# Performance work log

Measured on AMD Instinct MI355X. Metric: run time of the kernel, lower is better.

Reference implementation:

```python
import jax, jax.numpy as jnp
import numpy as np

FONT_NUM = 190
HID = 256
HEADS = 2
EPS = 1e-5


def _bn(x, g, b, m, v):
    # eval-mode BatchNorm over the last (channel) axis
    return (x - m) * (g * jax.lax.rsqrt(v + EPS)) + b


def _gru(x, Wih, Whh, bih, bhh):
    # x: [B, S, D]; PyTorch gate order r, z, n. Returns all hidden states [B, S, H].
    B, S, _ = x.shape
    H = Whh.shape[1]
    xp = x @ Wih.T + bih  # [B, S, 3H] -- one big GEMM for all timesteps
    def step(h, xt):
        gh = h @ Whh.T + bhh
        xr, xz, xn = jnp.split(xt, 3, axis=-1)
        hr, hz, hn = jnp.split(gh, 3, axis=-1)
        r = jax.nn.sigmoid(xr + hr)
        z = jax.nn.sigmoid(xz + hz)
        n = jnp.tanh(xn + r * hn)
        h_new = (1.0 - z) * n + z * h
        return h_new, h_new
    h0 = jnp.zeros((B, H), x.dtype)
    _, hs = jax.lax.scan(step, h0, jnp.swapaxes(xp, 0, 1))
    return jnp.swapaxes(hs, 0, 1)


def _forward(img_emb, text_embs, len_mask, label_mask, labels,
             img_W, img_b, img_g, img_beta, img_m, img_v,
             g1_Wih, g1_Whh, g1_bih, g1_bhh, tl_W, tl_b,
             t_g, t_beta, t_m, t_v,
             g2_Wih, g2_Whh, g2_bih, g2_bhh, cl_W, cl_b,
             c_g, c_beta, c_m, c_v,
             attn_Win, attn_bin, attn_Wout, attn_bout, pred_W, pred_b):
    # img encoder: Linear -> BN -> (Dropout eval=id) -> ReLU
    img_fea = jax.nn.relu(_bn(img_emb @ img_W.T + img_b, img_g, img_beta, img_m, img_v))  # [B,H]
    # text encoder: GRU -> ReLU -> Linear, then BN+ReLU (torch does this in [B,C,S]; equivalent over channels)
    t = jax.nn.relu(_gru(text_embs, g1_Wih, g1_Whh, g1_bih, g1_bhh))
    t = t @ tl_W.T + tl_b
    text_fea = jax.nn.relu(_bn(t, t_g, t_beta, t_m, t_v))  # [B,S,H]
    len_info = len_mask.sum(axis=1)  # [B]
    # NOTE: sum over ALL timesteps divided by valid length (faithful to source)
    mean = text_fea.sum(axis=1) / len_info[:, None]  # [B,H]
    contrast = text_fea - mean[:, None, :]
    c = jax.nn.relu(_gru(contrast, g2_Wih, g2_Whh, g2_bih, g2_bhh))
    c = c @ cl_W.T + cl_b
    contrast_fea = jax.nn.relu(_bn(c, c_g, c_beta, c_m, c_v))  # [B,S,H]
    B, S, H = text_fea.shape
    hd = H // HEADS
    # batched 3-token self-attention: collapse the per-timestep python loop into one call
    tokens = jnp.stack([
        jnp.broadcast_to(img_fea[:, None, :], (B, S, H)), text_fea, contrast_fea
    ], axis=0).reshape(3, B * S, H)  # [3, N, H]
    Wq, Wk, Wv = jnp.split(attn_Win, 3, axis=0)
    bq, bk, bv = jnp.split(attn_bin, 3, axis=0)
    scale = 1.0 / jnp.sqrt(jnp.asarray(hd, tokens.dtype))
    q = (tokens @ Wq.T + bq).reshape(3, B * S, HEADS, hd) * scale
    k = (tokens @ Wk.T + bk).reshape(3, B * S, HEADS, hd)
    v = (tokens @ Wv.T + bv).reshape(3, B * S, HEADS, hd)
    scores = jnp.einsum('tnhd,snhd->nhts', q, k)  # [N, heads, 3, 3]
    attn = jax.nn.softmax(scores, axis=-1)
    o = jnp.einsum('nhts,snhd->tnhd', attn, v).reshape(3, B * S, H)
    o = o @ attn_Wout.T + attn_bout
    last = o.mean(axis=0).reshape(B, S, H)  # att_fea.mean(0) over the 3 tokens
    logits = last @ pred_W.T + pred_b  # [B,S,FONT_NUM]
    pred = jax.nn.softmax(logits, axis=-1)
    oh = jnp.maximum(label_mask, jax.nn.one_hot(labels, FONT_NUM, dtype=pred.dtype))
    loss = -(oh * jnp.log(pred)).sum(axis=-1)  # [B,S]
    loss = (loss * len_mask).sum(axis=1) / len_info
    return loss.mean()


def setup_inputs() -> dict:
    key = jax.random.key(0)
    ks = jax.random.split(key, 16)
    B, S, D, H = 128, 128, 2048, HID
    img_emb = jax.random.normal(ks[0], (B, D), jnp.float32)
    text_embs = jax.random.normal(ks[1], (B, S, D), jnp.float32)
    lengths = jax.random.randint(ks[2], (B,), S // 2, S + 1)
    len_mask = (jnp.arange(S)[None, :] < lengths[:, None]).astype(jnp.float32)
    labels = jax.random.randint(ks[3], (B, S), 0, FONT_NUM)
    label_mask = jnp.zeros((B, S, FONT_NUM), jnp.float32)
    w = lambda k, sh: jax.random.normal(k, sh, jnp.float32) * 0.02
    params = dict(
        img_W=w(ks[4], (H, D)), img_b=jnp.zeros((H,)),
        img_g=jnp.ones((H,)), img_beta=jnp.zeros((H,)), img_m=jnp.zeros((H,)), img_v=jnp.ones((H,)),
        g1_Wih=w(ks[5], (3 * (H // 2), D)), g1_Whh=w(ks[6], (3 * (H // 2), H // 2)),
        g1_bih=jnp.zeros((3 * (H // 2),)), g1_bhh=jnp.zeros((3 * (H // 2),)),
        tl_W=w(ks[7], (H, H // 2)), tl_b=jnp.zeros((H,)),
        t_g=jnp.ones((H,)), t_beta=jnp.zeros((H,)), t_m=jnp.zeros((H,)), t_v=jnp.ones((H,)),
        g2_Wih=w(ks[8], (3 * H, H)), g2_Whh=w(ks[9], (3 * H, H)),
        g2_bih=jnp.zeros((3 * H,)), g2_bhh=jnp.zeros((3 * H,)),
        cl_W=w(ks[10], (H, H)), cl_b=jnp.zeros((H,)),
        c_g=jnp.ones((H,)), c_beta=jnp.zeros((H,)), c_m=jnp.zeros((H,)), c_v=jnp.ones((H,)),
        attn_Win=w(ks[11], (3 * H, H)), attn_bin=jnp.zeros((3 * H,)),
        attn_Wout=w(ks[12], (H, H)), attn_bout=jnp.zeros((H,)),
        pred_W=w(ks[13], (FONT_NUM, H)), pred_b=jnp.zeros((FONT_NUM,)),
    )
    return dict(img_emb=img_emb, text_embs=text_embs, len_mask=len_mask,
                label_mask=label_mask, labels=labels, **params)


def reference(img_emb, text_embs, len_mask, label_mask, labels,
              img_W, img_b, img_g, img_beta, img_m, img_v,
              g1_Wih, g1_Whh, g1_bih, g1_bhh, tl_W, tl_b,
              t_g, t_beta, t_m, t_v,
              g2_Wih, g2_Whh, g2_bih, g2_bhh, cl_W, cl_b,
              c_g, c_beta, c_m, c_v,
              attn_Win, attn_bin, attn_Wout, attn_bout, pred_W, pred_b):
    return _forward(img_emb, text_embs, len_mask, label_mask, labels,
                    img_W, img_b, img_g, img_beta, img_m, img_v,
                    g1_Wih, g1_Whh, g1_bih, g1_bhh, tl_W, tl_b,
                    t_g, t_beta, t_m, t_v,
                    g2_Wih, g2_Whh, g2_bih, g2_bhh, cl_W, cl_b,
                    c_g, c_beta, c_m, c_v,
                    attn_Win, attn_bin, attn_Wout, attn_bout, pred_W, pred_b)
```

## Files before the change

kernel.cpp:

```cpp
#include <hip/hip_runtime.h>

typedef __attribute__((ext_vector_type(8))) short short8;
typedef __attribute__((ext_vector_type(4))) float f32x4;
typedef _Float16 f16;
typedef __attribute__((ext_vector_type(2))) _Float16 f16x2;
typedef __attribute__((ext_vector_type(8))) _Float16 f16x8;

__device__ inline float bf2f(unsigned short u){
  union{float f; unsigned u32;} x; x.u32 = ((unsigned)u) << 16; return x.f;
}
__device__ inline unsigned short f2bf(float f){
  union{float f; unsigned u;} x; x.f = f;
  unsigned r = (x.u + 0x7FFFu + ((x.u >> 16) & 1u)) >> 16;
  return (unsigned short)r;
}

#if defined(__has_builtin)
#  if __has_builtin(__builtin_amdgcn_fdot2)
#    define HAS_FDOT2 1
#  endif
#endif
__device__ inline float dot2f(f16x2 a, f16x2 b, float c){
#ifdef HAS_FDOT2
  return __builtin_amdgcn_fdot2(a, b, c, false);
#else
  return c + (float)a.x * (float)b.x + (float)a.y * (float)b.y;
#endif
}
__device__ inline f16x2 asf16x2(int v){ return __builtin_bit_cast(f16x2, v); }
__device__ inline int pack2(float lo, float hi){
  f16x2 p = f16x2{(f16)lo, (f16)hi};
  return __builtin_bit_cast(int, p);
}

__device__ inline float sigmoidf_(float x){ return 1.f / (1.f + __expf(-x)); }
__device__ inline float tanh_fast(float x){ float e = __expf(2.f * x); return 1.f - 2.f / (e + 1.f); }

__device__ inline float dpp_xor1(float x){
  return __int_as_float(__builtin_amdgcn_update_dpp(0, __float_as_int(x), 0xB1, 0xF, 0xF, true));
}
__device__ inline float dpp_xor2(float x){
  return __int_as_float(__builtin_amdgcn_update_dpp(0, __float_as_int(x), 0x4E, 0xF, 0xF, true));
}

__device__ inline void load8bf(const unsigned short* p, float* o){
  uint4 q = *(const uint4*)p;
  o[0]=bf2f((unsigned short)(q.x & 0xffffu)); o[1]=bf2f((unsigned short)(q.x >> 16));
  o[2]=bf2f((unsigned short)(q.y & 0xffffu)); o[3]=bf2f((unsigned short)(q.y >> 16));
  o[4]=bf2f((unsigned short)(q.z & 0xffffu)); o[5]=bf2f((unsigned short)(q.z >> 16));
  o[6]=bf2f((unsigned short)(q.w & 0xffffu)); o[7]=bf2f((unsigned short)(q.w >> 16));
}

#define GLL16(g, l) __builtin_amdgcn_global_load_lds(                      \
    (const __attribute__((address_space(1))) void*)(g),                    \
    (__attribute__((address_space(3))) void*)(l), 16, 0, 0)

__global__ __launch_bounds__(256) void conv_bf16_k(const float* __restrict__ src,
                                                   unsigned short* __restrict__ dst, int n4){
  int i = blockIdx.x * 256 + threadIdx.x;
  if (i >= n4) return;
  float4 v = ((const float4*)src)[i];
  union { unsigned short s[4]; uint2 q; } u;
  u.s[0]=f2bf(v.x); u.s[1]=f2bf(v.y); u.s[2]=f2bf(v.z); u.s[3]=f2bf(v.w);
  ((uint2*)dst)[i] = u.q;
}

__global__ __launch_bounds__(256) void conv_f16_k(const float* __restrict__ src,
                                                  f16* __restrict__ dst, int n4){
  int i = blockIdx.x * 256 + threadIdx.x;
  if (i >= n4) return;
  float4 v = ((const float4*)src)[i];
  union { f16 s[4]; uint2 q; } u;
  u.s[0]=(f16)v.x; u.s[1]=(f16)v.y; u.s[2]=(f16)v.z; u.s[3]=(f16)v.w;
  ((uint2*)dst)[i] = u.q;
}

__global__ __launch_bounds__(256) void pred_pad_k(const float* __restrict__ W,
                                                  const float* __restrict__ b,
                                                  unsigned short* __restrict__ Wd,
                                                  float* __restrict__ bd){
  int i = blockIdx.x * 256 + threadIdx.x;
  int j = i >> 8;
  Wd[i] = (j < 190) ? f2bf(W[i]) : (unsigned short)0;
  if (i < 192) bd[i] = (i < 190) ? b[i] : 0.f;
}

template<int OUT_T, bool BN, bool AF32>
__global__ __launch_bounds__(256) void gemm128_k(
    const void* __restrict__ Ap, const unsigned short* __restrict__ Bw,
    const float* __restrict__ bias,
    const float* __restrict__ gam, const float* __restrict__ bet,
    const float* __restrict__ mu,  const float* __restrict__ var,
    void* __restrict__ Cp, int M, int N, int K)
{
  __shared__ __align__(16) unsigned short As[4096];
  __shared__ __align__(16) unsigned short Bs[4096];
  const int tid  = threadIdx.x;
  const int lane = tid & 63, wid = tid >> 6;
  const int wm = wid & 1, wn = wid >> 1;
  const int bm = blockIdx.y << 7, bn = blockIdx.x << 7;
  const int rA = tid >> 2, seg = tid & 3;

  f32x4 acc[4][4];
  #pragma unroll
  for (int i = 0; i < 4; i++)
    #pragma unroll
    for (int j = 0; j < 4; j++)
      acc[i][j] = f32x4{0.f, 0.f, 0.f, 0.f};

  const unsigned short* Abf = (const unsigned short*)Ap;
  const float* Af = (const float*)Ap;
  char* asb = (char*)As;
  char* bsb = (char*)Bs;
  char* asw = asb + wid * 1024;
  char* bsw = bsb + wid * 1024;

  for (int k0 = 0; k0 < K; k0 += 32) {
    if (AF32) {
      #pragma unroll
      for (int beta = 0; beta < 2; beta++) {
        const float* src = Af + (size_t)(bm + rA + beta * 64) * K + k0 + seg * 8;
        float4 v0 = *(const float4*)src;
        float4 v1 = *(const float4*)(src + 4);
        union { unsigned short s[8]; uint4 q; } u;
        u.s[0]=f2bf(v0.x); u.s[1]=f2bf(v0.y); u.s[2]=f2bf(v0.z); u.s[3]=f2bf(v0.w);
        u.s[4]=f2bf(v1.x); u.s[5]=f2bf(v1.y); u.s[6]=f2bf(v1.z); u.s[7]=f2bf(v1.w);
        *(uint4*)(asb + beta * 4096 + tid * 16) = u.q;
      }
    } else {
      GLL16(Abf + (size_t)(bm + rA)      * K + k0 + seg * 8, asw);
      GLL16(Abf + (size_t)(bm + rA + 64) * K + k0 + seg * 8, asw + 4096);
    }
    GLL16(Bw + (size_t)(bn + rA)      * K + k0 + seg * 8, bsw);
    GLL16(Bw + (size_t)(bn + rA + 64) * K + k0 + seg * 8, bsw + 4096);
    __syncthreads();

    short8 a[4], b[4];
    #pragma unroll
    for (int f = 0; f < 4; f++) {
      int ra = wm * 64 + f * 16 + (lane & 15);
      a[f] = *(const short8*)(asb + ra * 64 + (lane >> 4) * 16);
      int rb = wn * 64 + f * 16 + (lane & 15);
      b[f] = *(const short8*)(bsb + rb * 64 + (lane >> 4) * 16);
    }
    #pragma unroll
    for (int fm = 0; fm < 4; fm++)
      #pragma unroll
      for (int fn = 0; fn < 4; fn++)
        acc[fm][fn] = __builtin_amdgcn_mfma_f32_16x16x32_bf16(a[fm], b[fn], acc[fm][fn], 0, 0, 0);
    __syncthreads();
  }

  #pragma unroll
  for (int fn = 0; fn < 4; fn++) {
    int col = bn + wn * 64 + fn * 16 + (lane & 15);
    float bs = bias[col];
    float sc = 1.f, sh = 0.f;
    if (BN) { float s = gam[col] * rsqrtf(var[col] + 1e-5f); sc = s; sh = bet[col] - mu[col] * s; }
    #pragma unroll
    for (int fm = 0; fm < 4; fm++) {
      int row = bm + wm * 64 + fm * 16 + ((lane >> 4) << 2);
      #pragma unroll
      for (int j = 0; j < 4; j++) {
        float v = acc[fm][fn][j] + bs;
        if (BN) { v = v * sc + sh; v = fmaxf(v, 0.f); }
        size_t idx = (size_t)(row + j) * N + col;
        if (OUT_T == 1) ((f16*)Cp)[idx] = (f16)v;
        else            ((unsigned short*)Cp)[idx] = f2bf(v);
      }
    }
  }
}

template<int OUT_T, bool BN, bool AF32>
__global__ __launch_bounds__(256) void gemm_k(
    const void* __restrict__ Ap, const unsigned short* __restrict__ Bw,
    const float* __restrict__ bias,
    const float* __restrict__ gam, const float* __restrict__ bet,
    const float* __restrict__ mu,  const float* __restrict__ var,
    void* __restrict__ Cp, int M, int N, int K)
{
  __shared__ unsigned short As[64][40];
  __shared__ unsigned short Bs[64][40];
  const int tid  = threadIdx.x;
  const int lane = tid & 63, wid = tid >> 6;
  const int wm = wid & 1, wn = wid >> 1;
  const int bm = blockIdx.y << 6, bn = blockIdx.x << 6;
  const int srow = tid >> 2, sseg = tid & 3;

  f32x4 acc[2][2];
  #pragma unroll
  for (int i = 0; i < 2; i++)
    #pragma unroll
    for (int j = 0; j < 2; j++)
      acc[i][j] = f32x4{0.f, 0.f, 0.f, 0.f};

  const unsigned short* Abf = (const unsigned short*)Ap;
  const float* Af = (const float*)Ap;

  for (int k0 = 0; k0 < K; k0 += 32) {
    if (AF32) {
      const float* src = Af + (size_t)(bm + srow) * K + k0 + sseg * 8;
      float4 v0 = *(const float4*)(src);
      float4 v1 = *(const float4*)(src + 4);
      union { unsigned short s[8]; uint4 q; } u;
      u.s[0]=f2bf(v0.x); u.s[1]=f2bf(v0.y); u.s[2]=f2bf(v0.z); u.s[3]=f2bf(v0.w);
      u.s[4]=f2bf(v1.x); u.s[5]=f2bf(v1.y); u.s[6]=f2bf(v1.z); u.s[7]=f2bf(v1.w);
      *(uint4*)&As[srow][sseg * 8] = u.q;
    } else {
      *(uint4*)&As[srow][sseg * 8] =
          *(const uint4*)(Abf + (size_t)(bm + srow) * K + k0 + sseg * 8);
    }
    *(uint4*)&Bs[srow][sseg * 8] =
        *(const uint4*)(Bw + (size_t)(bn + srow) * K + k0 + sseg * 8);
    __syncthreads();

    short8 a0 = *(const short8*)&As[wm * 32 +      (lane & 15)][(lane >> 4) * 8];
    short8 a1 = *(const short8*)&As[wm * 32 + 16 + (lane & 15)][(lane >> 4) * 8];
    short8 b0 = *(const short8*)&Bs[wn * 32 +      (lane & 15)][(lane >> 4) * 8];
    short8 b1 = *(const short8*)&Bs[wn * 32 + 16 + (lane & 15)][(lane >> 4) * 8];
    acc[0][0] = __builtin_amdgcn_mfma_f32_16x16x32_bf16(a0, b0, acc[0][0], 0, 0, 0);
    acc[0][1] = __builtin_amdgcn_mfma_f32_16x16x32_bf16(a0, b1, acc[0][1], 0, 0, 0);
    acc[1][0] = __builtin_amdgcn_mfma_f32_16x16x32_bf16(a1, b0, acc[1][0], 0, 0, 0);
    acc[1][1] = __builtin_amdgcn_mfma_f32_16x16x32_bf16(a1, b1, acc[1][1], 0, 0, 0);
    __syncthreads();
  }

  #pragma unroll
  for (int fn = 0; fn < 2; fn++) {
    int col = bn + wn * 32 + fn * 16 + (lane & 15);
    float bs = bias[col];
    float sc = 1.f, sh = 0.f;
    if (BN) { float s = gam[col] * rsqrtf(var[col] + 1e-5f); sc = s; sh = bet[col] - mu[col] * s; }
    #pragma unroll
    for (int fm = 0; fm < 2; fm++) {
      int row = bm + wm * 32 + fm * 16 + ((lane >> 4) << 2);
      #pragma unroll
      for (int j = 0; j < 4; j++) {
        float v = acc[fm][fn][j] + bs;
        if (BN) { v = v * sc + sh; v = fmaxf(v, 0.f); }
        size_t idx = (size_t)(row + j) * N + col;
        if (OUT_T == 0)      ((float*)Cp)[idx] = v;
        else if (OUT_T == 1) ((f16*)Cp)[idx]   = (f16)v;
        else                 ((unsigned short*)Cp)[idx] = f2bf(v);
      }
    }
  }
}

__global__ __launch_bounds__(512, 2) void gru2_scan_k(
    const f16* __restrict__ Wf,
    const float* __restrict__ bhh,
    const f16* __restrict__ xp, unsigned short* __restrict__ hs_relu)
{
  const int b = blockIdx.x;
  const int tid = threadIdx.x;
  const int jj = tid >> 1, kh = tid & 1;
  __shared__ __align__(16) f16 hbuf[2][256];
  __shared__ __align__(16) char wnl[16 * 512 * 16];

  {
    const f16* src = Wf + (size_t)(512 + jj) * 256 + kh * 128;
    #pragma unroll
    for (int c = 0; c < 16; c++)
      *(uint4*)(wnl + c * 8192 + tid * 16) = *(const uint4*)(src + c * 8);
  }

  int wri[64], wzi[64];
  #pragma unroll
  for (int i = 0; i < 16; i++) {
    const int kb = kh * 128 + i * 8;
    uint4 q;
    q = *(const uint4*)&Wf[(size_t)(jj      ) * 256 + kb];
    wri[4*i+0] = (int)q.x; wri[4*i+1] = (int)q.y; wri[4*i+2] = (int)q.z; wri[4*i+3] = (int)q.w;
    q = *(const uint4*)&Wf[(size_t)(jj + 256) * 256 + kb];
    wzi[4*i+0] = (int)q.x; wzi[4*i+1] = (int)q.y; wzi[4*i+2] = (int)q.z; wzi[4*i+3] = (int)q.w;
  }
  #pragma unroll
  for (int i = 0; i < 64; i++)
    asm volatile("" : "+v"(wri[i]), "+v"(wzi[i]));

  const float br = bhh[jj], bz = bhh[jj + 256], bn2 = bhh[jj + 512];
  if (tid < 256) hbuf[0][tid] = (f16)0.f;
  float hprev = 0.f;
  f16 pxr = (f16)0.f, pxz = (f16)0.f, pxn = (f16)0.f;
  if (kh == 0) {
    const f16* x0 = xp + (size_t)(b * 128) * 768;
    pxr = x0[jj]; pxz = x0[256 + jj]; pxn = x0[512 + jj];
  }
  __syncthreads();
  int cur = 0;
  const char* mybase = wnl + tid * 16;
  for (int t = 0; t < 128; t++) {
    float xr = (float)pxr, xz = (float)pxz, xn = (float)pxn;
    if (kh == 0) {
      const int tn = (t < 127) ? (t + 1) : 127;
      const f16* xnr = xp + (size_t)(b * 128 + tn) * 768;
      pxr = xnr[jj]; pxz = xnr[256 + jj]; pxn = xnr[512 + jj];
    }
    const char* hb = (const char*)hbuf[cur] + kh * 256;
    float ar = 0.f, az = 0.f, an = 0.f;
    #pragma unroll
    for (int i = 0; i < 16; i++) {
      f16x8 hv = *(const f16x8*)(hb + i * 16);
      f16x8 wv = *(const f16x8*)(mybase + i * 8192);
      #pragma unroll
      for (int u = 0; u < 4; u++) {
        f16x2 hp = f16x2{hv[2*u], hv[2*u+1]};
        ar = dot2f(asf16x2(wri[4*i+u]), hp, ar);
        az = dot2f(asf16x2(wzi[4*i+u]), hp, az);
        an = dot2f(f16x2{wv[2*u], wv[2*u+1]}, hp, an);
      }
    }
    ar += dpp_xor1(ar);
    az += dpp_xor1(az);
    an += dpp_xor1(an);
    if (kh == 0) {
      float r = sigmoidf_(xr + ar + br);
      float z = sigmoidf_(xz + az + bz);
      float n = tanh_fast(xn + r * (an + bn2));
      float hnew = (1.f - z) * n + z * hprev;
      hprev = hnew;
      hbuf[cur ^ 1][jj] = (f16)hnew;
      hs_relu[(size_t)(b * 128 + t) * 256 + jj] = f2bf(fmaxf(hnew, 0.f));
    }
    __syncthreads();
    cur ^= 1;
  }
}

__global__ __launch_bounds__(512, 4) void gru1_scan_k(
    const float* __restrict__ Whh, const float* __restrict__ bhh,
    const f16* __restrict__ xp, unsigned short* __restrict__ hs_relu)
{
  const int b = blockIdx.x;
  const int tid = threadIdx.x;
  const int jj = tid >> 2, kh = tid & 3;
  __shared__ __align__(16) f16 hbuf[2][128];

  int wri[16], wzi[16], wni[16];
  #pragma unroll
  for (int i = 0; i < 4; i++) {
    const int kb = kh * 32 + i * 8;
    float4 f0, f1;
    f0 = *(const float4*)&Whh[(size_t)(jj      ) * 128 + kb];
    f1 = *(const float4*)&Whh[(size_t)(jj      ) * 128 + kb + 4];
    wri[4*i+0] = pack2(f0.x, f0.y); wri[4*i+1] = pack2(f0.z, f0.w);
    wri[4*i+2] = pack2(f1.x, f1.y); wri[4*i+3] = pack2(f1.z, f1.w);
    f0 = *(const float4*)&Whh[(size_t)(jj + 128) * 128 + kb];
    f1 = *(const float4*)&Whh[(size_t)(jj + 128) * 128 + kb + 4];
    wzi[4*i+0] = pack2(f0.x, f0.y); wzi[4*i+1] = pack2(f0.z, f0.w);
    wzi[4*i+2] = pack2(f1.x, f1.y); wzi[4*i+3] = pack2(f1.z, f1.w);
    f0 = *(const float4*)&Whh[(size_t)(jj + 256) * 128 + kb];
    f1 = *(const float4*)&Whh[(size_t)(jj + 256) * 128 + kb + 4];
    wni[4*i+0] = pack2(f0.x, f0.y); wni[4*i+1] = pack2(f0.z, f0.w);
    wni[4*i+2] = pack2(f1.x, f1.y); wni[4*i+3] = pack2(f1.z, f1.w);
  }
  #pragma unroll
  for (int i = 0; i < 16; i++)
    asm volatile("" : "+v"(wri[i]), "+v"(wzi[i]), "+v"(wni[i]));

  const float br = bhh[jj], bz = bhh[jj + 128], bn2 = bhh[jj + 256];
  if (tid < 128) hbuf[0][tid] = (f16)0.f;
  float hprev = 0.f;
  f16 pxr = (f16)0.f, pxz = (f16)0.f, pxn = (f16)0.f;
  if (kh == 0) {
    const f16* x0 = xp + (size_t)(b * 128) * 384;
    pxr = x0[jj]; pxz = x0[128 + jj]; pxn = x0[256 + jj];
  }
  __syncthreads();
  int cur = 0;
  for (int t = 0; t < 128; t++) {
    float xr = (float)pxr, xz = (float)pxz, xn = (float)pxn;
    if (kh == 0) {
      const int tn = (t < 127) ? (t + 1) : 127;
      const f16* xnr = xp + (size_t)(b * 128 + tn) * 384;
      pxr = xnr[jj]; pxz = xnr[128 + jj]; pxn = xnr[256 + jj];
    }
    const char* hb = (const char*)hbuf[cur] + kh * 64;
    float ar = 0.f, az = 0.f, an = 0.f;
    #pragma unroll
    for (int c = 0; c < 4; c++) {
      f16x8 hv = *(const f16x8*)(hb + c * 16);
      #pragma unroll
      for (int u = 0; u < 4; u++) {
        f16x2 hp = f16x2{hv[2*u], hv[2*u+1]};
        ar = dot2f(asf16x2(wri[4*c+u]), hp, ar);
        az = dot2f(asf16x2(wzi[4*c+u]), hp, az);
        an = dot2f(asf16x2(wni[4*c+u]), hp, an);
      }
    }
    ar += dpp_xor1(ar); ar += dpp_xor2(ar);
    az += dpp_xor1(az); az += dpp_xor2(az);
    an += dpp_xor1(an); an += dpp_xor2(an);
    if (kh == 0) {
      float r = sigmoidf_(xr + ar + br);
      float z = sigmoidf_(xz + az + bz);
      float n = tanh_fast(xn + r * (an + bn2));
      float hnew = (1.f - z) * n + z * hprev;
      hprev = hnew;
      hbuf[cur ^ 1][jj] = (f16)hnew;
      hs_relu[(size_t)(b * 128 + t) * 128 + jj] = f2bf(fmaxf(hnew, 0.f));
    }
    __syncthreads();
    cur ^= 1;
  }
}

__global__ __launch_bounds__(256) void mean_k(const unsigned short* __restrict__ tf,
                                              const float* __restrict__ len_mask,
                                              float* __restrict__ mean,
                                              float* __restrict__ len_info){
  int b = blockIdx.x, c = threadIdx.x;
  float acc = 0.f;
  for (int s = 0; s < 128; s++) acc += bf2f(tf[(size_t)(b * 128 + s) * 256 + c]);
  float len = 0.f;
  for (int s = 0; s < 128; s++) len += len_mask[b * 128 + s];
  mean[b * 256 + c] = acc / len;
  if (c == 0) len_info[b] = len;
}

__global__ __launch_bounds__(256) void contrast_k(const unsigned short* __restrict__ tf,
                                                  const float* __restrict__ mean,
                                                  unsigned short* __restrict__ out){
  size_t i = (size_t)blockIdx.x * 256 + threadIdx.x;
  int c = (int)(i & 255);
  int b = (int)(i >> 15);
  out[i] = f2bf(bf2f(tf[i]) - mean[b * 256 + c]);
}

__global__ __launch_bounds__(256) void attn_k(const unsigned short* __restrict__ qkv0,
                                              const unsigned short* __restrict__ qkv1,
                                              const unsigned short* __restrict__ qkv2,
                                              unsigned short* __restrict__ osum){
  int i = blockIdx.x * 256 + threadIdx.x;
  int h = i & 1; int n = i >> 1; int b = n >> 7;
  const unsigned short* t0 = qkv0 + (size_t)b * 768 + h * 128;
  const unsigned short* t1 = qkv1 + (size_t)n * 768 + h * 128;
  const unsigned short* t2 = qkv2 + (size_t)n * 768 + h * 128;
  float sc[3][3];
  #pragma unroll
  for (int a = 0; a < 3; a++)
    #pragma unroll
    for (int s = 0; s < 3; s++) sc[a][s] = 0.f;
  #pragma unroll 1
  for (int dc = 0; dc < 16; dc++) {
    float q[3][8], k[3][8];
    load8bf(t0 + dc * 8, q[0]); load8bf(t1 + dc * 8, q[1]); load8bf(t2 + dc * 8, q[2]);
    load8bf(t0 + 256 + dc * 8, k[0]); load8bf(t1 + 256 + dc * 8, k[1]); load8bf(t2 + 256 + dc * 8, k[2]);
    #pragma unroll
    for (int a = 0; a < 3; a++)
      #pragma unroll
      for (int s = 0; s < 3; s++) {
        float d = 0.f;
        #pragma unroll
        for (int e = 0; e < 8; e++) d += q[a][e] * k[s][e];
        sc[a][s] += d;
      }
  }
  const float scale = 0.08838834764831845f;
  float w[3] = {0.f, 0.f, 0.f};
  #pragma unroll
  for (int a = 0; a < 3; a++) {
    float s0 = sc[a][0] * scale, s1 = sc[a][1] * scale, s2 = sc[a][2] * scale;
    float m = fmaxf(s0, fmaxf(s1, s2));
    float e0 = __expf(s0 - m), e1 = __expf(s1 - m), e2 = __expf(s2 - m);
    float inv = 1.f / (e0 + e1 + e2);
    w[0] += e0 * inv; w[1] += e1 * inv; w[2] += e2 * inv;
  }
  w[0] *= (1.f / 3.f); w[1] *= (1.f / 3.f); w[2] *= (1.f / 3.f);
  unsigned short* op = osum + (size_t)n * 256 + h * 128;
  #pragma unroll 1
  for (int dc = 0; dc < 16; dc++) {
    float v0[8], v1[8], v2[8];
    load8bf(t0 + 512 + dc * 8, v0); load8bf(t1 + 512 + dc * 8, v1); load8bf(t2 + 512 + dc * 8, v2);
    union { unsigned short s[8]; uint4 q; } u;
    #pragma unroll
    for (int e = 0; e < 8; e++) u.s[e] = f2bf(w[0] * v0[e] + w[1] * v1[e] + w[2] * v2[e]);
    *(uint4*)(op + dc * 8) = u.q;
  }
}

__global__ __launch_bounds__(64) void loss_k(const float* __restrict__ logits,
                                             const float* __restrict__ label_mask,
                                             const int* __restrict__ labels,
                                             float* __restrict__ loss_raw){
  int r = blockIdx.x; int j = threadIdx.x;
  int lab = labels[r];
  float l[3]; float m = -1e30f;
  #pragma unroll
  for (int q = 0; q < 3; q++) {
    int c = j + q * 64;
    float lv = (c < 190) ? logits[(size_t)r * 192 + c] : -1e30f;
    l[q] = lv; m = fmaxf(m, lv);
  }
  #pragma unroll
  for (int off = 32; off; off >>= 1) m = fmaxf(m, __shfl_xor(m, off));
  float se = 0.f, soh = 0.f, dot = 0.f;
  #pragma unroll
  for (int q = 0; q < 3; q++) {
    int c = j + q * 64;
    if (c < 190) {
      se += expf(l[q] - m);
      float oh = fmaxf(label_mask[(size_t)r * 190 + c], (c == lab) ? 1.f : 0.f);
      soh += oh; dot += oh * l[q];
    }
  }
  #pragma unroll
  for (int off = 32; off; off >>= 1) {
    se += __shfl_xor(se, off); soh += __shfl_xor(soh, off); dot += __shfl_xor(dot, off);
  }
  if (j == 0) loss_raw[r] = (m + logf(se)) * soh - dot;
}

__global__ __launch_bounds__(256) void final_k(const float* __restrict__ loss_raw,
                                               const float* __restrict__ len_mask,
                                               const float* __restrict__ len_info,
                                               float* __restrict__ out){
  __shared__ float sh[256];
  int t = threadIdx.x;
  float acc = 0.f;
  for (int i = t; i < 16384; i += 256) acc += loss_raw[i] * len_mask[i] / len_info[i >> 7];
  sh[t] = acc; __syncthreads();
  for (int s = 128; s; s >>= 1) { if (t < s) sh[t] += sh[t + s]; __syncthreads(); }
  if (t == 0) out[0] = sh[0] / 128.f;
}

extern "C" void kernel_launch(void* const* d_in, const int* in_sizes, int n_in,
                              void* d_out, int out_size, void* d_ws, size_t ws_size,
                              hipStream_t stream)
{
  const float* img_emb    = (const float*)d_in[0];
  const float* text_embs  = (const float*)d_in[1];
  const float* len_mask   = (const float*)d_in[2];
  const float* label_mask = (const float*)d_in[3];
  const int*   labels     = (const int*)  d_in[4];
  const float* img_W   = (const float*)d_in[5];
  const float* img_b   = (const float*)d_in[6];
  const float* img_g   = (const float*)d_in[7];
  const float* img_be  = (const float*)d_in[8];
  const float* img_m   = (const float*)d_in[9];
  const float* img_v   = (const float*)d_in[10];
  const float* g1_Wih  = (const float*)d_in[11];
  const float* g1_Whh  = (const float*)d_in[12];
  const float* g1_bih  = (const float*)d_in[13];
  const float* g1_bhh  = (const float*)d_in[14];
  const float* tl_W    = (const float*)d_in[15];
  const float* tl_b    = (const float*)d_in[16];
  const float* t_g     = (const float*)d_in[17];
  const float* t_be    = (const float*)d_in[18];
  const float* t_m     = (const float*)d_in[19];
  const float* t_v     = (const float*)d_in[20];
  const float* g2_Wih  = (const float*)d_in[21];
  const float* g2_Whh  = (const float*)d_in[22];
  const float* g2_bih  = (const float*)d_in[23];
  const float* g2_bhh  = (const float*)d_in[24];
  const float* cl_W    = (const float*)d_in[25];
  const float* cl_b    = (const float*)d_in[26];
  const float* c_g     = (const float*)d_in[27];
  const float* c_be    = (const float*)d_in[28];
  const float* c_m     = (const float*)d_in[29];
  const float* c_v     = (const float*)d_in[30];
  const float* a_Win   = (const float*)d_in[31];
  const float* a_bin   = (const float*)d_in[32];
  const float* a_Wout  = (const float*)d_in[33];
  const float* a_bout  = (const float*)d_in[34];
  const float* pred_W  = (const float*)d_in[35];
  const float* pred_b  = (const float*)d_in[36];

  char* ws = (char*)d_ws;
  size_t o = 0;
  auto alloc = [&](size_t sz){ size_t r = o; o += (sz + 255) & ~(size_t)255; return r; };

  size_t o_g1Wih = alloc(384ull*2048*2);
  size_t o_tlW   = alloc(256ull*128*2);
  size_t o_g2Wih = alloc(768ull*256*2);
  size_t o_g2Whh = alloc(768ull*256*2);
  size_t o_clW   = alloc(256ull*256*2);
  size_t o_aWin  = alloc(768ull*256*2);
  size_t o_aWout = alloc(256ull*256*2);
  size_t o_imgW  = alloc(256ull*2048*2);
  size_t o_predW = alloc(192ull*256*2);
  size_t o_predb = alloc(192ull*4);
  size_t o_imgfea= alloc(128ull*256*2);
  size_t o_mean  = alloc(128ull*256*4);
  size_t o_len   = alloc(128ull*4);
  size_t o_R0    = alloc(33554432ull);
  size_t o_RB    = alloc(25165824ull);
  size_t o_tfea  = alloc(16384ull*256*2);
  size_t o_qkv1  = alloc(16384ull*768*2);
  size_t o_cfea  = alloc(16384ull*256*2);
  size_t o_qkv0  = alloc(128ull*768*2);
  size_t o_loss  = alloc(16384ull*4);
  (void)ws_size; (void)in_sizes; (void)n_in; (void)out_size;

  unsigned short* g1Wih_bf = (unsigned short*)(ws + o_g1Wih);
  unsigned short* tlW_bf   = (unsigned short*)(ws + o_tlW);
  unsigned short* g2Wih_bf = (unsigned short*)(ws + o_g2Wih);
  f16*            g2Whh_f  = (f16*)(ws + o_g2Whh);
  unsigned short* clW_bf   = (unsigned short*)(ws + o_clW);
  unsigned short* aWin_bf  = (unsigned short*)(ws + o_aWin);
  unsigned short* aWout_bf = (unsigned short*)(ws + o_aWout);
  unsigned short* imgW_bf  = (unsigned short*)(ws + o_imgW);
  unsigned short* predW_bf = (unsigned short*)(ws + o_predW);
  float*          predb_p  = (float*)(ws + o_predb);
  unsigned short* img_fea  = (unsigned short*)(ws + o_imgfea);
  float*          meanb    = (float*)(ws + o_mean);
  float*          len_info = (float*)(ws + o_len);
  f16*            xp2      = (f16*)(ws + o_R0);
  unsigned short* hs2      = (unsigned short*)(ws + o_R0 + 25165824ull);
  unsigned short* osum     = (unsigned short*)(ws + o_R0);
  unsigned short* lastb    = (unsigned short*)(ws + o_R0 + 8388608ull);
  f16*            xp1      = (f16*)(ws + o_RB);
  unsigned short* hs1      = (unsigned short*)(ws + o_RB + 12582912ull);
  unsigned short* contr    = (unsigned short*)(ws + o_RB + 16777216ull);
  unsigned short* qkv2     = (unsigned short*)(ws + o_RB);
  unsigned short* tfea     = (unsigned short*)(ws + o_tfea);
  unsigned short* qkv1     = (unsigned short*)(ws + o_qkv1);
  float*          logits   = (float*)(ws + o_qkv1);
  unsigned short* cfea     = (unsigned short*)(ws + o_cfea);
  unsigned short* qkv0     = (unsigned short*)(ws + o_qkv0);
  float*          loss_raw = (float*)(ws + o_loss);
  float*          outp     = (float*)d_out;

  conv_bf16_k<<<768, 256, 0, stream>>>(g1_Wih, g1Wih_bf, 196608);
  conv_bf16_k<<<32,  256, 0, stream>>>(tl_W,   tlW_bf,   8192);
  conv_bf16_k<<<192, 256, 0, stream>>>(g2_Wih, g2Wih_bf, 49152);
  conv_f16_k <<<192, 256, 0, stream>>>(g2_Whh, g2Whh_f,  49152);
  conv_bf16_k<<<64,  256, 0, stream>>>(cl_W,   clW_bf,   16384);
  conv_bf16_k<<<192, 256, 0, stream>>>(a_Win,  aWin_bf,  49152);
  conv_bf16_k<<<64,  256, 0, stream>>>(a_Wout, aWout_bf, 16384);
  conv_bf16_k<<<512, 256, 0, stream>>>(img_W,  imgW_bf,  131072);
  pred_pad_k<<<192, 256, 0, stream>>>(pred_W, pred_b, predW_bf, predb_p);

  gemm128_k<2, true, true><<<dim3(2, 1), 256, 0, stream>>>(
      img_emb, imgW_bf, img_b, img_g, img_be, img_m, img_v, img_fea, 128, 256, 2048);

  gemm128_k<1, false, true><<<dim3(3, 128), 256, 0, stream>>>(
      text_embs, g1Wih_bf, g1_bih, nullptr, nullptr, nullptr, nullptr, xp1, 16384, 384, 2048);

  gru1_scan_k<<<128, 512, 0, stream>>>(g1_Whh, g1_bhh, xp1, hs1);

  gemm128_k<2, true, false><<<dim3(2, 128), 256, 0, stream>>>(
      hs1, tlW_bf, tl_b, t_g, t_be, t_m, t_v, tfea, 16384, 256, 128);

  mean_k<<<128, 256, 0, stream>>>(tfea, len_mask, meanb, len_info);
  contrast_k<<<16384, 256, 0, stream>>>(tfea, meanb, contr);

  gemm128_k<1, false, false><<<dim3(6, 128), 256, 0, stream>>>(
      contr, g2Wih_bf, g2_bih, nullptr, nullptr, nullptr, nullptr, xp2, 16384, 768, 256);

  gru2_scan_k<<<128, 512, 0, stream>>>(g2Whh_f, g2_bhh, xp2, hs2);

  gemm128_k<2, true, false><<<dim3(2, 128), 256, 0, stream>>>(
      hs2, clW_bf, cl_b, c_g, c_be, c_m, c_v, cfea, 16384, 256, 256);

  gemm128_k<2, false, false><<<dim3(6, 1), 256, 0, stream>>>(
      img_fea, aWin_bf, a_bin, nullptr, nullptr, nullptr, nullptr, qkv0, 128, 768, 256);
  gemm128_k<2, false, false><<<dim3(6, 128), 256, 0, stream>>>(
      tfea, aWin_bf, a_bin, nullptr, nullptr, nullptr, nullptr, qkv1, 16384, 768, 256);
  gemm128_k<2, false, false><<<dim3(6, 128), 256, 0, stream>>>(
      cfea, aWin_bf, a_bin, nullptr, nullptr, nullptr, nullptr, qkv2, 16384, 768, 256);

  attn_k<<<128, 256, 0, stream>>>(qkv0, qkv1, qkv2, osum);

  gemm128_k<2, false, false><<<dim3(2, 128), 256, 0, stream>>>(
      osum, aWout_bf, a_bout, nullptr, nullptr, nullptr, nullptr, lastb, 16384, 256, 256);

  gemm_k<0, false, false><<<dim3(3, 256), 256, 0, stream>>>(
      lastb, predW_bf, predb_p, nullptr, nullptr, nullptr, nullptr, logits, 16384, 192, 256);

  loss_k<<<16384, 64, 0, stream>>>(logits, label_mask, labels, loss_raw);
  final_k<<<1, 256, 0, stream>>>(loss_raw, len_mask, len_info, outp);
}
```

Baseline: 625.2 us.

## Fuse contrast subtraction into GRU2 input GEMM and merge weight conversions

Removes the standalone contrast kernel by subtracting the per-batch mean while staging A tiles in the GRU2 input-projection GEMM (new A_MODE 2), avoiding a write and re-read of an 8MB intermediate. The eight weight-conversion launches are also merged into a single kernel that dispatches by index range, cutting launch overhead. The fused A path uses register loads and conversion instead of direct global-to-LDS loads, which adds some ALU work to each GEMM k-step.

After: 619.9 us. No clear change (-0.9%).

```diff
diff --git a/kernel.cpp b/kernel.cpp
--- a/kernel.cpp
+++ b/kernel.cpp
@@ -55,24 +55,37 @@
     (const __attribute__((address_space(1))) void*)(g),                    \
     (__attribute__((address_space(3))) void*)(l), 16, 0, 0)
 
-__global__ __launch_bounds__(256) void conv_bf16_k(const float* __restrict__ src,
-                                                   unsigned short* __restrict__ dst, int n4){
+__global__ __launch_bounds__(256) void conv_all_k(
+    const float* __restrict__ s0, const float* __restrict__ s1,
+    const float* __restrict__ s2, const float* __restrict__ s3,
+    const float* __restrict__ s4, const float* __restrict__ s5,
+    const float* __restrict__ s6, const float* __restrict__ s7,
+    unsigned short* __restrict__ d0, unsigned short* __restrict__ d1,
+    unsigned short* __restrict__ d2, f16* __restrict__ d3,
+    unsigned short* __restrict__ d4, unsigned short* __restrict__ d5,
+    unsigned short* __restrict__ d6, unsigned short* __restrict__ d7)
+{
   int i = blockIdx.x * 256 + threadIdx.x;
-  if (i >= n4) return;
-  float4 v = ((const float4*)src)[i];
-  union { unsigned short s[4]; uint2 q; } u;
-  u.s[0]=f2bf(v.x); u.s[1]=f2bf(v.y); u.s[2]=f2bf(v.z); u.s[3]=f2bf(v.w);
-  ((uint2*)dst)[i] = u.q;
-}
-
-__global__ __launch_bounds__(256) void conv_f16_k(const float* __restrict__ src,
-                                                  f16* __restrict__ dst, int n4){
-  int i = blockIdx.x * 256 + threadIdx.x;
-  if (i >= n4) return;
-  float4 v = ((const float4*)src)[i];
-  union { f16 s[4]; uint2 q; } u;
-  u.s[0]=(f16)v.x; u.s[1]=(f16)v.y; u.s[2]=(f16)v.z; u.s[3]=(f16)v.w;
-  ((uint2*)dst)[i] = u.q;
+  if (i >= 516096) return;
+  const float* src; int local; int mode = 0; unsigned short* dst = nullptr; f16* dstf = nullptr;
+  if (i < 196608)      { src = s0; local = i;           dst = d0; }
+  else if (i < 204800) { src = s1; local = i - 196608;  dst = d1; }
+  else if (i < 253952) { src = s2; local = i - 204800;  dst = d2; }
+  else if (i < 303104) { src = s3; local = i - 253952;  dstf = d3; mode = 1; }
+  else if (i < 319488) { src = s4; local = i - 303104;  dst = d4; }
+  else if (i < 368640) { src = s5; local = i - 319488;  dst = d5; }
+  else if (i < 385024) { src = s6; local = i - 368640;  dst = d6; }
+  else                 { src = s7; local = i - 385024;  dst = d7; }
+  float4 v = ((const float4*)src)[local];
+  if (mode == 0) {
+    union { unsigned short s[4]; uint2 q; } u;
+    u.s[0]=f2bf(v.x); u.s[1]=f2bf(v.y); u.s[2]=f2bf(v.z); u.s[3]=f2bf(v.w);
+    ((uint2*)dst)[local] = u.q;
+  } else {
+    union { f16 s[4]; uint2 q; } u;
+    u.s[0]=(f16)v.x; u.s[1]=(f16)v.y; u.s[2]=(f16)v.z; u.s[3]=(f16)v.w;
+    ((uint2*)dstf)[local] = u.q;
+  }
 }
 
 __global__ __launch_bounds__(256) void pred_pad_k(const float* __restrict__ W,
@@ -85,7 +98,7 @@
   if (i < 192) bd[i] = (i < 190) ? b[i] : 0.f;
 }
 
-template<int OUT_T, bool BN, bool AF32>
+template<int OUT_T, bool BN, int A_MODE>
 __global__ __launch_bounds__(256) void gemm128_k(
     const void* __restrict__ Ap, const unsigned short* __restrict__ Bw,
     const float* __restrict__ bias,
@@ -116,7 +129,7 @@
   char* bsw = bsb + wid * 1024;
 
   for (int k0 = 0; k0 < K; k0 += 32) {
-    if (AF32) {
+    if (A_MODE == 1) {
       #pragma unroll
       for (int beta = 0; beta < 2; beta++) {
         const float* src = Af + (size_t)(bm + rA + beta * 64) * K + k0 + seg * 8;
@@ -125,6 +138,20 @@
         union { unsigned short s[8]; uint4 q; } u;
         u.s[0]=f2bf(v0.x); u.s[1]=f2bf(v0.y); u.s[2]=f2bf(v0.z); u.s[3]=f2bf(v0.w);
         u.s[4]=f2bf(v1.x); u.s[5]=f2bf(v1.y); u.s[6]=f2bf(v1.z); u.s[7]=f2bf(v1.w);
+        *(uint4*)(asb + beta * 4096 + tid * 16) = u.q;
+      }
+    } else if (A_MODE == 2) {
+      const float* mrow = mu + (size_t)(bm >> 7) * 256 + k0 + seg * 8;
+      float4 m0 = *(const float4*)mrow;
+      float4 m1 = *(const float4*)(mrow + 4);
+      #pragma unroll
+      for (int beta = 0; beta < 2; beta++) {
+        const unsigned short* src = Abf + (size_t)(bm + rA + beta * 64) * K + k0 + seg * 8;
+        float av[8];
+        load8bf(src, av);
+        union { unsigned short s[8]; uint4 q; } u;
+        u.s[0]=f2bf(av[0]-m0.x); u.s[1]=f2bf(av[1]-m0.y); u.s[2]=f2bf(av[2]-m0.z); u.s[3]=f2bf(av[3]-m0.w);
+        u.s[4]=f2bf(av[4]-m1.x); u.s[5]=f2bf(av[5]-m1.y); u.s[6]=f2bf(av[6]-m1.z); u.s[7]=f2bf(av[7]-m1.w);
         *(uint4*)(asb + beta * 4096 + tid * 16) = u.q;
       }
     } else {
@@ -418,15 +445,6 @@
   for (int s = 0; s < 128; s++) len += len_mask[b * 128 + s];
   mean[b * 256 + c] = acc / len;
   if (c == 0) len_info[b] = len;
-}
-
-__global__ __launch_bounds__(256) void contrast_k(const unsigned short* __restrict__ tf,
-                                                  const float* __restrict__ mean,
-                                                  unsigned short* __restrict__ out){
-  size_t i = (size_t)blockIdx.x * 256 + threadIdx.x;
-  int c = (int)(i & 255);
-  int b = (int)(i >> 15);
-  out[i] = f2bf(bf2f(tf[i]) - mean[b * 256 + c]);
 }
 
 __global__ __launch_bounds__(256) void attn_k(const unsigned short* __restrict__ qkv0,
@@ -613,7 +631,6 @@
   unsigned short* lastb    = (unsigned short*)(ws + o_R0 + 8388608ull);
   f16*            xp1      = (f16*)(ws + o_RB);
   unsigned short* hs1      = (unsigned short*)(ws + o_RB + 12582912ull);
-  unsigned short* contr    = (unsigned short*)(ws + o_RB + 16777216ull);
   unsigned short* qkv2     = (unsigned short*)(ws + o_RB);
   unsigned short* tfea     = (unsigned short*)(ws + o_tfea);
   unsigned short* qkv1     = (unsigned short*)(ws + o_qkv1);
@@ -623,48 +640,42 @@
   float*          loss_raw = (float*)(ws + o_loss);
   float*          outp     = (float*)d_out;
 
-  conv_bf16_k<<<768, 256, 0, stream>>>(g1_Wih, g1Wih_bf, 196608);
-  conv_bf16_k<<<32,  256, 0, stream>>>(tl_W,   tlW_bf,   8192);
-  conv_bf16_k<<<192, 256, 0, stream>>>(g2_Wih, g2Wih_bf, 49152);
-  conv_f16_k <<<192, 256, 0, stream>>>(g2_Whh, g2Whh_f,  49152);
-  conv_bf16_k<<<64,  256, 0, stream>>>(cl_W,   clW_bf,   16384);
-  conv_bf16_k<<<192, 256, 0, stream>>>(a_Win,  aWin_bf,  49152);
-  conv_bf16_k<<<64,  256, 0, stream>>>(a_Wout, aWout_bf, 16384);
-  conv_bf16_k<<<512, 256, 0, stream>>>(img_W,  imgW_bf,  131072);
+  conv_all_k<<<2016, 256, 0, stream>>>(
+      g1_Wih, tl_W, g2_Wih, g2_Whh, cl_W, a_Win, a_Wout, img_W,
+      g1Wih_bf, tlW_bf, g2Wih_bf, g2Whh_f, clW_bf, aWin_bf, aWout_bf, imgW_bf);
   pred_pad_k<<<192, 256, 0, stream>>>(pred_W, pred_b, predW_bf, predb_p);
 
-  gemm128_k<2, true, true><<<dim3(2, 1), 256, 0, stream>>>(
+  gemm128_k<2, true, 1><<<dim3(2, 1), 256, 0, stream>>>(
       img_emb, imgW_bf, img_b, img_g, img_be, img_m, img_v, img_fea, 128, 256, 2048);
 
-  gemm128_k<1, false, true><<<dim3(3, 128), 256, 0, stream>>>(
+  gemm128_k<1, false, 1><<<dim3(3, 128), 256, 0, stream>>>(
       text_embs, g1Wih_bf, g1_bih, nullptr, nullptr, nullptr, nullptr, xp1, 16384, 384, 2048);
 
   gru1_scan_k<<<128, 512, 0, stream>>>(g1_Whh, g1_bhh, xp1, hs1);
 
-  gemm128_k<2, true, false><<<dim3(2, 128), 256, 0, stream>>>(
+  gemm128_k<2, true, 0><<<dim3(2, 128), 256, 0, stream>>>(
       hs1, tlW_bf, tl_b, t_g, t_be, t_m, t_v, tfea, 16384, 256, 128);
 
   mean_k<<<128, 256, 0, stream>>>(tfea, len_mask, meanb, len_info);
-  contrast_k<<<16384, 256, 0, stream>>>(tfea, meanb, contr);
-
-  gemm128_k<1, false, false><<<dim3(6, 128), 256, 0, stream>>>(
-      contr, g2Wih_bf, g2_bih, nullptr, nullptr, nullptr, nullptr, xp2, 16384, 768, 256);
+
+  gemm128_k<1, false, 2><<<dim3(6, 128), 256, 0, stream>>>(
+      tfea, g2Wih_bf, g2_bih, nullptr, nullptr, meanb, nullptr, xp2, 16384, 768, 256);
 
   gru2_scan_k<<<128, 512, 0, stream>>>(g2Whh_f, g2_bhh, xp2, hs2);
 
-  gemm128_k<2, true, false><<<dim3(2, 128), 256, 0, stream>>>(
+  gemm128_k<2, true, 0><<<dim3(2, 128), 256, 0, stream>>>(
       hs2, clW_bf, cl_b, c_g, c_be, c_m, c_v, cfea, 16384, 256, 256);
 
-  gemm128_k<2, false, false><<<dim3(6, 1), 256, 0, stream>>>(
+  gemm128_k<2, false, 0><<<dim3(6, 1), 256, 0, stream>>>(
       img_fea, aWin_bf, a_bin, nullptr, nullptr, nullptr, nullptr, qkv0, 128, 768, 256);
-  gemm128_k<2, false, false><<<dim3(6, 128), 256, 0, stream>>>(
+  gemm128_k<2, false, 0><<<dim3(6, 128), 256, 0, stream>>>(
       tfea, aWin_bf, a_bin, nullptr, nullptr, nullptr, nullptr, qkv1, 16384, 768, 256);
-  gemm128_k<2, false, false><<<dim3(6, 128), 256, 0, stream>>>(
+  gemm128_k<2, false, 0><<<dim3(6, 128), 256, 0, stream>>>(
       cfea, aWin_bf, a_bin, nullptr, nullptr, nullptr, nullptr, qkv2, 16384, 768, 256);
 
   attn_k<<<128, 256, 0, stream>>>(qkv0, qkv1, qkv2, osum);
 
-  gemm128_k<2, false, false><<<dim3(2, 128), 256, 0, stream>>>(
+  gemm128_k<2, false, 0><<<dim3(2, 128), 256, 0, stream>>>(
       osum, aWout_bf, a_bout, nullptr, nullptr, nullptr, nullptr, lastb, 16384, 256, 256);
 
   gemm_k<0, false, false><<<dim3(3, 256), 256, 0, stream>>>(
```
